# Kernel optimization log

Measured on AMD Instinct MI355X. Metric: run time of the kernel, lower is better.

Reference implementation:

```python
import jax, jax.numpy as jnp
import numpy as np
import math

T, B, E, H = 1024, 4, 512, 8
HD = E // H

def setup_inputs() -> dict:
    key = jax.random.key(0)
    ks = jax.random.split(key, 6)
    return {
        "query": jax.random.normal(ks[0], (T, B, E), dtype=jnp.float32),
        "dist": jax.random.normal(ks[1], (B, T, T, H), dtype=jnp.float32) * 0.1,
        "in_proj_weight": jax.random.normal(ks[2], (3 * E, E), dtype=jnp.float32) * 0.02,
        "in_proj_bias": jax.random.normal(ks[3], (3 * E,), dtype=jnp.float32) * 0.02,
        "out_proj_weight": jax.random.normal(ks[4], (E, E), dtype=jnp.float32) * 0.02,
        "out_proj_bias": jax.random.normal(ks[5], (E,), dtype=jnp.float32) * 0.02,
    }

def reference(query, dist, in_proj_weight, in_proj_bias, out_proj_weight, out_proj_bias):
    t, b, e = query.shape
    # packed in-projection (self-attention: q=k=v=query)
    qkv = query @ in_proj_weight.T + in_proj_bias          # [T,B,3E]
    q, k, v = jnp.split(qkv, 3, axis=-1)                   # each [T,B,E]
    def heads(x):
        return x.reshape(t, b * H, HD).transpose(1, 0, 2)  # [B*H,T,HD]
    q, k, v = heads(q), heads(k), heads(v)
    q = q / math.sqrt(HD)
    attn = jnp.einsum('bte,bse->bts', q, k)                # [B*H,T,T]
    # distance/structure bias: [B,T,T,H] -> [B,H,T,T] -> [B*H,T,T]
    bias = jnp.transpose(dist, (0, 3, 1, 2)).reshape(b * H, t, t)
    attn = jax.nn.softmax(attn + bias, axis=-1)
    out = jnp.einsum('bts,bse->bte', attn, v)              # [B*H,T,HD]
    out = out.transpose(1, 0, 2).reshape(t, b, e)          # [T,B,E]
    out = out @ out_proj_weight.T + out_proj_bias
    return out
```

## Files before the change

### kernel.cpp

```cpp
#include <hip/hip_runtime.h>
#include <math.h>

typedef __bf16 bf16;
typedef bf16 bf16x8 __attribute__((ext_vector_type(8)));
typedef bf16 bf16x4 __attribute__((ext_vector_type(4)));
typedef float f32x4 __attribute__((ext_vector_type(4)));

#define T_DIM 1024
#define B_DIM 4
#define E_DIM 512
#define H_DIM 8
#define HD_DIM 64
#define BH_DIM 32

__device__ __forceinline__ f32x4 mfma16(bf16x8 a, bf16x8 b, f32x4 c) {
    return __builtin_amdgcn_mfma_f32_16x16x32_bf16(a, b, c, 0, 0, 0);
}

__device__ __forceinline__ bf16x4 cvt4(f32x4 v) {
    bf16x4 o;
    o[0] = (bf16)v[0]; o[1] = (bf16)v[1]; o[2] = (bf16)v[2]; o[3] = (bf16)v[3];
    return o;
}

#define CVT_Q_V   524288
#define CVT_W1_V  196608
__global__ __launch_bounds__(256)
void cvt_all(const float* __restrict__ q, const float* __restrict__ w1,
             const float* __restrict__ w2, bf16* __restrict__ qo,
             bf16* __restrict__ w1o, bf16* __restrict__ w2o) {
    long v = (long)blockIdx.x * 256 + threadIdx.x;
    const float* src; bf16* dst;
    if (v < CVT_Q_V)                { src = q;  dst = qo; }
    else if (v < CVT_Q_V + CVT_W1_V){ v -= CVT_Q_V;  src = w1; dst = w1o; }
    else                            { v -= CVT_Q_V + CVT_W1_V; src = w2; dst = w2o; }
    f32x4 f = *(const f32x4*)(src + v * 4);
    *(bf16x4*)(dst + v * 4) = cvt4(f);
}

template<int TM, int TN, int MODE>
__global__ __launch_bounds__(256)
void gemm_t(const bf16* __restrict__ A, const bf16* __restrict__ Bt,
            const float* __restrict__ bias, int K, int N,
            float* __restrict__ out, bf16* __restrict__ qb,
            bf16* __restrict__ kb, bf16* __restrict__ vb) {
    constexpr int FM = TM / 32, FN = TN / 32;
    __shared__ __align__(16) bf16 As[TM * 72];
    __shared__ __align__(16) bf16 Bs[TN * 72];
    const int tid  = threadIdx.x;
    const int lane = tid & 63;
    const int wave = tid >> 6;
    const int quad = lane >> 4;
    const int l15  = lane & 15;
    const int wm = wave & 1, wn = wave >> 1;
    const int m0 = blockIdx.x * TM, n0 = blockIdx.y * TN;

    f32x4 acc[FM][FN] = {};

    const int sr = tid >> 2;
    const int sc = (tid & 3) * 16;

    for (int k0 = 0; k0 < K; k0 += 64) {
#pragma unroll
        for (int p = 0; p < TM / 64; p++) {
            const bf16* src = &A[(long)(m0 + p * 64 + sr) * K + k0 + sc];
            *(bf16x8*)&As[(p * 64 + sr) * 72 + sc]     = *(const bf16x8*)(src);
            *(bf16x8*)&As[(p * 64 + sr) * 72 + sc + 8] = *(const bf16x8*)(src + 8);
        }
#pragma unroll
        for (int p = 0; p < TN / 64; p++) {
            const bf16* src = &Bt[(long)(n0 + p * 64 + sr) * K + k0 + sc];
            *(bf16x8*)&Bs[(p * 64 + sr) * 72 + sc]     = *(const bf16x8*)(src);
            *(bf16x8*)&Bs[(p * 64 + sr) * 72 + sc + 8] = *(const bf16x8*)(src + 8);
        }
        __syncthreads();
#pragma unroll
        for (int kk = 0; kk < 64; kk += 32) {
            bf16x8 af[FM], bf[FN];
#pragma unroll
            for (int mb = 0; mb < FM; mb++)
                af[mb] = *(const bf16x8*)&As[(wm * (TM / 2) + mb * 16 + l15) * 72 + kk + quad * 8];
#pragma unroll
            for (int nb = 0; nb < FN; nb++)
                bf[nb] = *(const bf16x8*)&Bs[(wn * (TN / 2) + nb * 16 + l15) * 72 + kk + quad * 8];
#pragma unroll
            for (int mb = 0; mb < FM; mb++)
#pragma unroll
                for (int nb = 0; nb < FN; nb++)
                    acc[mb][nb] = mfma16(af[mb], bf[nb], acc[mb][nb]);
        }
        __syncthreads();
    }

#pragma unroll
    for (int mb = 0; mb < FM; mb++) {
#pragma unroll
        for (int nb = 0; nb < FN; nb++) {
            int n = n0 + wn * (TN / 2) + nb * 16 + l15;
            float bv = bias[n];
#pragma unroll
            for (int r = 0; r < 4; r++) {
                int m = m0 + wm * (TM / 2) + mb * 16 + quad * 4 + r;
                float v = acc[mb][nb][r] + bv;
                if (MODE == 0) {
                    out[(long)m * N + n] = v;
                } else {
                    int t = m >> 2, b = m & 3;
                    int sec = n >> 9, j = n & 511;
                    int h = j >> 6, hd = j & 63;
                    int bh = b * 8 + h;
                    if (sec == 0)
                        qb[((long)bh * T_DIM + t) * HD_DIM + hd] = (bf16)(v * 0.125f);
                    else if (sec == 1)
                        kb[((long)bh * T_DIM + t) * HD_DIM + hd] = (bf16)v;
                    else
                        vb[((long)bh * HD_DIM + hd) * T_DIM + t] = (bf16)v;
                }
            }
        }
    }
}

__global__ __launch_bounds__(256)
void attn_kernel(const bf16* __restrict__ qb, const bf16* __restrict__ kb,
                 const bf16* __restrict__ vb, const float* __restrict__ dist,
                 bf16* __restrict__ ctxb) {
    __shared__ __align__(16) bf16 Ks[64 * 72];
    __shared__ __align__(16) bf16 Vts[64 * 72];
    __shared__ __align__(16) bf16 Ps[4 * 16 * 72];
    const int tid  = threadIdx.x;
    const int lane = tid & 63;
    const int wave = tid >> 6;
    const int quad = lane >> 4;
    const int l15  = lane & 15;
    const int bid = blockIdx.x;
    const int bh  = bid >> 4;
    const int qt  = bid & 15;
    const int b   = bh >> 3, h = bh & 7;
    const int qrow = qt * 64 + wave * 16 + l15;

    bf16x8 qa0 = *(const bf16x8*)&qb[((long)bh * T_DIM + qrow) * HD_DIM + quad * 8];
    bf16x8 qa1 = *(const bf16x8*)&qb[((long)bh * T_DIM + qrow) * HD_DIM + 32 + quad * 8];

    f32x4 oacc[4] = {};
    float lsum[4] = {0.f, 0.f, 0.f, 0.f};

    const int r0 = tid >> 3;
    const int c0 = (tid & 7) * 8;

    const float* dp = dist + (long)(b * 1024 + qt * 64 + wave * 16 + quad * 4) * 8192 + h;

    bf16x8 pk0, pk1, pv0, pv1;
    float pbias[16];
    pk0 = *(const bf16x8*)&kb[((long)bh * T_DIM + r0) * HD_DIM + c0];
    pk1 = *(const bf16x8*)&kb[((long)bh * T_DIM + r0 + 32) * HD_DIM + c0];
    pv0 = *(const bf16x8*)&vb[((long)bh * HD_DIM + r0) * T_DIM + c0];
    pv1 = *(const bf16x8*)&vb[((long)bh * HD_DIM + r0 + 32) * T_DIM + c0];
#pragma unroll
    for (int r = 0; r < 4; r++)
#pragma unroll
        for (int nb = 0; nb < 4; nb++)
            pbias[r * 4 + nb] = dp[(long)r * 8192 + (nb * 16 + l15) * 8];

    for (int st = 0; st < T_DIM; st += 64) {
        __syncthreads();
        *(bf16x8*)&Ks[r0 * 72 + c0]         = pk0;
        *(bf16x8*)&Ks[(r0 + 32) * 72 + c0]  = pk1;
        *(bf16x8*)&Vts[r0 * 72 + c0]        = pv0;
        *(bf16x8*)&Vts[(r0 + 32) * 72 + c0] = pv1;
        __syncthreads();

        if (st + 64 < T_DIM) {
            const int sn = st + 64;
            pk0 = *(const bf16x8*)&kb[((long)bh * T_DIM + sn + r0) * HD_DIM + c0];
            pk1 = *(const bf16x8*)&kb[((long)bh * T_DIM + sn + r0 + 32) * HD_DIM + c0];
            pv0 = *(const bf16x8*)&vb[((long)bh * HD_DIM + r0) * T_DIM + sn + c0];
            pv1 = *(const bf16x8*)&vb[((long)bh * HD_DIM + r0 + 32) * T_DIM + sn + c0];
        }

        f32x4 sacc[4] = {};
        __builtin_amdgcn_s_setprio(1);
#pragma unroll
        for (int kk = 0; kk < 64; kk += 32) {
            bf16x8 a = (kk == 0) ? qa0 : qa1;
#pragma unroll
            for (int nb = 0; nb < 4; nb++) {
                bf16x8 bfr = *(const bf16x8*)&Ks[(nb * 16 + l15) * 72 + kk + quad * 8];
                sacc[nb] = mfma16(a, bfr, sacc[nb]);
            }
        }
        __builtin_amdgcn_s_setprio(0);

        bf16* pw = &Ps[wave * 16 * 72];
#pragma unroll
        for (int r = 0; r < 4; r++) {
            float rs = 0.f;
#pragma unroll
            for (int nb = 0; nb < 4; nb++) {
                float p = __expf(sacc[nb][r] + pbias[r * 4 + nb]);
                rs += p;
                pw[(quad * 4 + r) * 72 + nb * 16 + l15] = (bf16)p;
            }
            lsum[r] += rs;
        }

        if (st + 64 < T_DIM) {
            const int sn = st + 64;
#pragma unroll
            for (int r = 0; r < 4; r++)
#pragma unroll
                for (int nb = 0; nb < 4; nb++)
                    pbias[r * 4 + nb] = dp[(long)r * 8192 + (sn + nb * 16 + l15) * 8];
        }

        __builtin_amdgcn_s_setprio(1);
#pragma unroll
        for (int kk = 0; kk < 64; kk += 32) {
            bf16x8 ap = *(const bf16x8*)&pw[l15 * 72 + kk + quad * 8];
#pragma unroll
            for (int nb = 0; nb < 4; nb++) {
                bf16x8 bv2 = *(const bf16x8*)&Vts[(nb * 16 + l15) * 72 + kk + quad * 8];
                oacc[nb] = mfma16(ap, bv2, oacc[nb]);
            }
        }
        __builtin_amdgcn_s_setprio(0);
    }

#pragma unroll
    for (int r = 0; r < 4; r++) {
#pragma unroll
        for (int msk = 1; msk < 16; msk <<= 1)
            lsum[r] += __shfl_xor(lsum[r], msk);
    }

#pragma unroll
    for (int nb = 0; nb < 4; nb++) {
#pragma unroll
        for (int r = 0; r < 4; r++) {
            int t  = qt * 64 + wave * 16 + quad * 4 + r;
            int hd = nb * 16 + l15;
            float o = oacc[nb][r] / lsum[r];
            ctxb[((long)t * B_DIM + b) * E_DIM + h * HD_DIM + hd] = (bf16)o;
        }
    }
}

extern "C" void kernel_launch(void* const* d_in, const int* in_sizes, int n_in,
                              void* d_out, int out_size, void* d_ws, size_t ws_size,
                              hipStream_t stream) {
    const float* query = (const float*)d_in[0];
    const float* dist  = (const float*)d_in[1];
    const float* win   = (const float*)d_in[2];
    const float* bin   = (const float*)d_in[3];
    const float* wout  = (const float*)d_in[4];
    const float* bout  = (const float*)d_in[5];
    float* out = (float*)d_out;

    bf16* qb   = (bf16*)d_ws;
    bf16* kb   = qb + (1 << 21);
    bf16* vb   = kb + (1 << 21);
    bf16* qbf  = vb + (1 << 21);
    bf16* w1bf = qbf + (1 << 21);
    bf16* w2bf = w1bf + 786432;
    bf16* ctxb = w2bf + 262144;

    cvt_all<<<dim3(3072), 256, 0, stream>>>(query, win, wout, qbf, w1bf, w2bf);
    gemm_t<128, 128, 1><<<dim3(32, 12), 256, 0, stream>>>(
        qbf, w1bf, bin, 512, 1536, nullptr, qb, kb, vb);
    attn_kernel<<<dim3(512), 256, 0, stream>>>(qb, kb, vb, dist, ctxb);
    gemm_t<128, 64, 0><<<dim3(32, 8), 256, 0, stream>>>(
        ctxb, w2bf, bout, 512, 512, out, nullptr, nullptr, nullptr);
}
```

Measured before the change: 280.6 us.

## Split attention over key dimension into 4 partial blocks with combine kernel

Splits the key/value sequence of the attention kernel into four chunks, so the grid grows from 512 to 2048 blocks. Each block writes unnormalized fp32 partial outputs and row sums, and a new combine kernel adds them up, normalizes and writes the bf16 context. The intent is to fill the many compute units on the MI355X, which 512 blocks may leave underused. In exchange it adds about 32 MB of fp32 partial writes and reads plus an extra launch. Merging without a running max is safe because the original also skipped max subtraction.

```diff
diff --git a/kernel.cpp b/kernel.cpp
--- a/kernel.cpp
+++ b/kernel.cpp
@@ -12,6 +12,8 @@
 #define H_DIM 8
 #define HD_DIM 64
 #define BH_DIM 32
+#define SPLIT 4
+#define S_PER (T_DIM / SPLIT)
 
 __device__ __forceinline__ f32x4 mfma16(bf16x8 a, bf16x8 b, f32x4 c) {
     return __builtin_amdgcn_mfma_f32_16x16x32_bf16(a, b, c, 0, 0, 0);
@@ -124,7 +126,7 @@
 __global__ __launch_bounds__(256)
 void attn_kernel(const bf16* __restrict__ qb, const bf16* __restrict__ kb,
                  const bf16* __restrict__ vb, const float* __restrict__ dist,
-                 bf16* __restrict__ ctxb) {
+                 float* __restrict__ po, float* __restrict__ pl) {
     __shared__ __align__(16) bf16 Ks[64 * 72];
     __shared__ __align__(16) bf16 Vts[64 * 72];
     __shared__ __align__(16) bf16 Ps[4 * 16 * 72];
@@ -133,10 +135,12 @@
     const int wave = tid >> 6;
     const int quad = lane >> 4;
     const int l15  = lane & 15;
-    const int bid = blockIdx.x;
-    const int bh  = bid >> 4;
-    const int qt  = bid & 15;
-    const int b   = bh >> 3, h = bh & 7;
+    const int bid  = blockIdx.x;
+    const int bh   = (bid >> 4) & 31;
+    const int qt   = bid & 15;
+    const int split = bid >> 9;
+    const int s0   = split * S_PER;
+    const int b    = bh >> 3, h = bh & 7;
     const int qrow = qt * 64 + wave * 16 + l15;
 
     bf16x8 qa0 = *(const bf16x8*)&qb[((long)bh * T_DIM + qrow) * HD_DIM + quad * 8];
@@ -152,17 +156,17 @@
 
     bf16x8 pk0, pk1, pv0, pv1;
     float pbias[16];
-    pk0 = *(const bf16x8*)&kb[((long)bh * T_DIM + r0) * HD_DIM + c0];
-    pk1 = *(const bf16x8*)&kb[((long)bh * T_DIM + r0 + 32) * HD_DIM + c0];
-    pv0 = *(const bf16x8*)&vb[((long)bh * HD_DIM + r0) * T_DIM + c0];
-    pv1 = *(const bf16x8*)&vb[((long)bh * HD_DIM + r0 + 32) * T_DIM + c0];
+    pk0 = *(const bf16x8*)&kb[((long)bh * T_DIM + s0 + r0) * HD_DIM + c0];
+    pk1 = *(const bf16x8*)&kb[((long)bh * T_DIM + s0 + r0 + 32) * HD_DIM + c0];
+    pv0 = *(const bf16x8*)&vb[((long)bh * HD_DIM + r0) * T_DIM + s0 + c0];
+    pv1 = *(const bf16x8*)&vb[((long)bh * HD_DIM + r0 + 32) * T_DIM + s0 + c0];
 #pragma unroll
     for (int r = 0; r < 4; r++)
 #pragma unroll
         for (int nb = 0; nb < 4; nb++)
-            pbias[r * 4 + nb] = dp[(long)r * 8192 + (nb * 16 + l15) * 8];
-
-    for (int st = 0; st < T_DIM; st += 64) {
+            pbias[r * 4 + nb] = dp[(long)r * 8192 + (s0 + nb * 16 + l15) * 8];
+
+    for (int st = s0; st < s0 + S_PER; st += 64) {
         __syncthreads();
         *(bf16x8*)&Ks[r0 * 72 + c0]         = pk0;
         *(bf16x8*)&Ks[(r0 + 32) * 72 + c0]  = pk1;
@@ -170,7 +174,7 @@
         *(bf16x8*)&Vts[(r0 + 32) * 72 + c0] = pv1;
         __syncthreads();
 
-        if (st + 64 < T_DIM) {
+        if (st + 64 < s0 + S_PER) {
             const int sn = st + 64;
             pk0 = *(const bf16x8*)&kb[((long)bh * T_DIM + sn + r0) * HD_DIM + c0];
             pk1 = *(const bf16x8*)&kb[((long)bh * T_DIM + sn + r0 + 32) * HD_DIM + c0];
@@ -204,7 +208,7 @@
             lsum[r] += rs;
         }
 
-        if (st + 64 < T_DIM) {
+        if (st + 64 < s0 + S_PER) {
             const int sn = st + 64;
 #pragma unroll
             for (int r = 0; r < 4; r++)
@@ -233,16 +237,44 @@
             lsum[r] += __shfl_xor(lsum[r], msk);
     }
 
+    float* pob = po + (long)split * (BH_DIM * T_DIM * HD_DIM);
 #pragma unroll
     for (int nb = 0; nb < 4; nb++) {
 #pragma unroll
         for (int r = 0; r < 4; r++) {
             int t  = qt * 64 + wave * 16 + quad * 4 + r;
             int hd = nb * 16 + l15;
-            float o = oacc[nb][r] / lsum[r];
-            ctxb[((long)t * B_DIM + b) * E_DIM + h * HD_DIM + hd] = (bf16)o;
-        }
-    }
+            pob[((long)bh * T_DIM + t) * HD_DIM + hd] = oacc[nb][r];
+        }
+    }
+    if (l15 == 0) {
+#pragma unroll
+        for (int r = 0; r < 4; r++) {
+            int t = qt * 64 + wave * 16 + quad * 4 + r;
+            pl[(long)split * (BH_DIM * T_DIM) + bh * T_DIM + t] = lsum[r];
+        }
+    }
+}
+
+__global__ __launch_bounds__(256)
+void combine(const float* __restrict__ po, const float* __restrict__ pl,
+             bf16* __restrict__ ctxb) {
+    const int gid = blockIdx.x * 256 + threadIdx.x;
+    const int hd4 = gid & 15;
+    const int t   = (gid >> 4) & 1023;
+    const int bh  = gid >> 14;
+    const long base = ((long)bh * T_DIM + t) * HD_DIM + hd4 * 4;
+    f32x4 o = {};
+    float l = 0.f;
+#pragma unroll
+    for (int s = 0; s < SPLIT; s++) {
+        o += *(const f32x4*)&po[(long)s * (BH_DIM * T_DIM * HD_DIM) + base];
+        l += pl[(long)s * (BH_DIM * T_DIM) + bh * T_DIM + t];
+    }
+    float inv = 1.f / l;
+    f32x4 r = o * inv;
+    const int b = bh >> 3, hh = bh & 7;
+    *(bf16x4*)&ctxb[((long)t * B_DIM + b) * E_DIM + hh * HD_DIM + hd4 * 4] = cvt4(r);
 }
 
 extern "C" void kernel_launch(void* const* d_in, const int* in_sizes, int n_in,
@@ -263,11 +295,14 @@
     bf16* w1bf = qbf + (1 << 21);
     bf16* w2bf = w1bf + 786432;
     bf16* ctxb = w2bf + 262144;
+    float* po  = (float*)(ctxb + (1 << 21));
+    float* pl  = po + (long)SPLIT * BH_DIM * T_DIM * HD_DIM;
 
     cvt_all<<<dim3(3072), 256, 0, stream>>>(query, win, wout, qbf, w1bf, w2bf);
     gemm_t<128, 128, 1><<<dim3(32, 12), 256, 0, stream>>>(
         qbf, w1bf, bin, 512, 1536, nullptr, qb, kb, vb);
-    attn_kernel<<<dim3(512), 256, 0, stream>>>(qb, kb, vb, dist, ctxb);
+    attn_kernel<<<dim3(512 * SPLIT), 256, 0, stream>>>(qb, kb, vb, dist, po, pl);
+    combine<<<dim3(2048), 256, 0, stream>>>(po, pl, ctxb);
     gemm_t<128, 64, 0><<<dim3(32, 8), 256, 0, stream>>>(
         ctxb, w2bf, bout, 512, 512, out, nullptr, nullptr, nullptr);
 }
```

Result: slower. 295.6 us (+5.4%).
